# Performance work log

Hardware: AMD Instinct MI355X
Metric: run time of the kernel (lower is better)

Reference implementation:

```python
import jax, jax.numpy as jnp
import numpy as np

NUM_USERS = 100000
NUM_ITEMS = 50000
N_NODES = NUM_USERS + NUM_ITEMS
LATENT_DIM = 64
SBERT_DIM = 384
NUM_LAYERS = 3
N_EDGES = 2_000_000


def setup_inputs() -> dict:
    key = jax.random.key(0)
    k1, k2, k3, k4 = jax.random.split(key, 4)
    edge_index = jax.random.randint(k1, (2, N_EDGES), 0, N_NODES, dtype=jnp.int32)
    user_emb = jax.random.normal(k2, (NUM_USERS, LATENT_DIM), dtype=jnp.float32) * 0.1
    book_bert = jax.random.normal(k3, (NUM_ITEMS, SBERT_DIM), dtype=jnp.float32)
    # torch Linear weight layout: [out_features, in_features]
    w_proj = jax.random.normal(k4, (LATENT_DIM, SBERT_DIM), dtype=jnp.float32) * (1.0 / np.sqrt(SBERT_DIM))
    return {"edge_index": edge_index, "user_emb": user_emb, "book_bert": book_bert, "w_proj": w_proj}


def reference(edge_index, user_emb, book_bert, w_proj):
    src, dst = edge_index[0], edge_index[1]
    # initial embeddings: [users ; proj(book_bert)] -> [N, D]
    book_emb = book_bert @ w_proj.T
    emb0 = jnp.concatenate([user_emb, book_emb], axis=0)

    # symmetric gcn_norm without self-loops (PyG LGConv default)
    ones = jnp.ones((src.shape[0],), dtype=emb0.dtype)
    deg = jax.ops.segment_sum(ones, dst, num_segments=N_NODES)
    dis = jnp.where(deg > 0, jax.lax.rsqrt(jnp.maximum(deg, 1.0)), 0.0)
    norm = dis[src] * dis[dst]  # [E]

    x = emb0
    acc = emb0
    for _ in range(NUM_LAYERS):
        # out[dst] += norm * x[src]  (gather-scatter SpMM)
        msgs = norm[:, None] * x[src]  # [E, D]
        x = jax.ops.segment_sum(msgs, dst, num_segments=N_NODES)
        acc = acc + x
    out = acc / jnp.asarray(NUM_LAYERS + 1, dtype=emb0.dtype)
    return (emb0, out)
```

## Files before the change

kernel.cpp:

```cpp
#include <hip/hip_runtime.h>
#include <hip/hip_bf16.h>
#include <stdint.h>

#define NUM_USERS 100000
#define NUM_ITEMS 50000
#define N_NODES   150000
#define LATENT    64
#define SBERT     384
#define N_EDGES   2000000
#define OUT_OFF   (N_NODES * LATENT)
#define NBUCK     586
#define BCAP      4096
#define EPB       8192

typedef __hip_bfloat16 bf16;

__device__ __forceinline__ int ufl(int v) { return __builtin_amdgcn_readfirstlane(v); }

__global__ void k_zero_bcnt(int* __restrict__ bcnt) {
    int i = blockIdx.x * 256 + threadIdx.x;
    if (i < NBUCK) bcnt[i] = 0;
}

__global__ __launch_bounds__(256) void k_bin(const int* __restrict__ src,
                                             const int* __restrict__ dst,
                                             int* __restrict__ bcnt,
                                             unsigned* __restrict__ bin) {
    __shared__ int hist[NBUCK];
    __shared__ int base[NBUCK];
    const int tid = threadIdx.x;
    for (int i = tid; i < NBUCK; i += 256) hist[i] = 0;
    __syncthreads();
    const int e0 = blockIdx.x * EPB;
    const int e1 = min(e0 + EPB, N_EDGES);
    for (int e = e0 + tid; e < e1; e += 256)
        atomicAdd(&hist[dst[e] >> 8], 1);
    __syncthreads();
    for (int i = tid; i < NBUCK; i += 256) {
        int c = hist[i];
        base[i] = c ? atomicAdd(&bcnt[i], c) : 0;
        hist[i] = 0;
    }
    __syncthreads();
    for (int e = e0 + tid; e < e1; e += 256) {
        int d = dst[e];
        int b = d >> 8;
        int p = base[b] + atomicAdd(&hist[b], 1);
        bin[(size_t)b * BCAP + p] = (unsigned)src[e] | ((unsigned)(d & 255) << 18);
    }
}

__global__ __launch_bounds__(1024) void k_bscan(const int* __restrict__ bcnt,
                                                int* __restrict__ bbase) {
    __shared__ int sm[1024];
    int tid = threadIdx.x;
    int v = (tid < NBUCK) ? bcnt[tid] : 0;
    sm[tid] = v;
    __syncthreads();
    for (int off = 1; off < 1024; off <<= 1) {
        int t = (tid >= off) ? sm[tid - off] : 0;
        __syncthreads();
        sm[tid] += t;
        __syncthreads();
    }
    if (tid <= NBUCK) bbase[tid] = (tid == 0) ? 0 : sm[tid - 1];
}

__global__ __launch_bounds__(256) void k_build(const unsigned* __restrict__ bin,
                                               const int* __restrict__ bcnt,
                                               const int* __restrict__ bbase,
                                               int* __restrict__ rp,
                                               float* __restrict__ dis,
                                               int* __restrict__ cws) {
    __shared__ int h[256];
    __shared__ int lc[256];
    const int tid   = threadIdx.x;
    const int b     = blockIdx.x;
    const int nbase = b << 8;
    const unsigned* mybin = bin + (size_t)b * BCAP;
    h[tid] = 0;
    __syncthreads();
    const int cnt  = bcnt[b];
    const int base = bbase[b];
    for (int i = tid; i < cnt; i += 256)
        atomicAdd(&h[mybin[i] >> 18], 1);
    __syncthreads();
    int v = h[tid];
    __shared__ int sm[256];
    sm[tid] = v;
    __syncthreads();
    for (int off = 1; off < 256; off <<= 1) {
        int t = (tid >= off) ? sm[tid - off] : 0;
        __syncthreads();
        sm[tid] += t;
        __syncthreads();
    }
    int excl = sm[tid] - v;
    int n = nbase + tid;
    if (n < N_NODES) {
        rp[n]  = base + excl;
        dis[n] = (v > 0) ? rsqrtf((float)v) : 0.0f;
    }
    lc[tid] = base + excl;
    if (b == NBUCK - 1 && tid == 0) rp[N_NODES] = N_EDGES;
    __syncthreads();
    for (int i = tid; i < cnt; i += 256) {
        unsigned rec = mybin[i];
        int dl = rec >> 18;
        int pos = atomicAdd(&lc[dl], 1);
        cws[pos] = (int)(rec & 0x3FFFF);
    }
}

__global__ void k_copy_user(const float* __restrict__ u, const float* __restrict__ dis,
                            float* __restrict__ out, bf16* __restrict__ y) {
    int i = blockIdx.x * 256 + threadIdx.x;
    if (i < NUM_USERS * LATENT) {
        float v = u[i];
        out[i] = v;
        out[OUT_OFF + i] = v;
        float d = dis[i >> 6];
        y[i] = __float2bfloat16(d * v);
    }
}

__global__ __launch_bounds__(256) void k_proj(const float* __restrict__ bert,
                                              const float* __restrict__ w,
                                              const float* __restrict__ dis,
                                              float* __restrict__ out,
                                              bf16* __restrict__ y) {
    __shared__ float sB[128][33];
    __shared__ float sW[32][64];
    const int tid  = threadIdx.x;
    const int rb   = blockIdx.x * 128;
    const int col8 = (tid & 7) * 8;
    const int rowg = (tid >> 3) * 4;

    float acc[4][8];
#pragma unroll
    for (int i = 0; i < 4; ++i)
#pragma unroll
        for (int j = 0; j < 8; ++j) acc[i][j] = 0.0f;

    for (int kb = 0; kb < SBERT; kb += 32) {
        __syncthreads();
#pragma unroll
        for (int j = 0; j < 4; ++j) {
            int idx = tid + j * 256;
            int r  = idx >> 3;
            int k4 = (idx & 7) * 4;
            int rr = min(rb + r, NUM_ITEMS - 1);
            float4 v = *(const float4*)(bert + (size_t)rr * SBERT + kb + k4);
            sB[r][k4 + 0] = v.x; sB[r][k4 + 1] = v.y;
            sB[r][k4 + 2] = v.z; sB[r][k4 + 3] = v.w;
        }
#pragma unroll
        for (int j = 0; j < 2; ++j) {
            int idx = tid + j * 256;
            int c  = idx >> 3;
            int k4 = (idx & 7) * 4;
            float4 v = *(const float4*)(w + (size_t)c * SBERT + kb + k4);
            sW[k4 + 0][c] = v.x; sW[k4 + 1][c] = v.y;
            sW[k4 + 2][c] = v.z; sW[k4 + 3][c] = v.w;
        }
        __syncthreads();
#pragma unroll
        for (int kk = 0; kk < 32; ++kk) {
            float4 w0 = *(const float4*)&sW[kk][col8];
            float4 w1 = *(const float4*)&sW[kk][col8 + 4];
#pragma unroll
            for (int i = 0; i < 4; ++i) {
                float a = sB[rowg + i][kk];
                acc[i][0] = fmaf(a, w0.x, acc[i][0]);
                acc[i][1] = fmaf(a, w0.y, acc[i][1]);
                acc[i][2] = fmaf(a, w0.z, acc[i][2]);
                acc[i][3] = fmaf(a, w0.w, acc[i][3]);
                acc[i][4] = fmaf(a, w1.x, acc[i][4]);
                acc[i][5] = fmaf(a, w1.y, acc[i][5]);
                acc[i][6] = fmaf(a, w1.z, acc[i][6]);
                acc[i][7] = fmaf(a, w1.w, acc[i][7]);
            }
        }
    }
#pragma unroll
    for (int i = 0; i < 4; ++i) {
        int r = rb + rowg + i;
        if (r < NUM_ITEMS) {
            int n = NUM_USERS + r;
            size_t o = (size_t)n * LATENT + col8;
            float d = dis[n];
            float4 f0 = make_float4(acc[i][0], acc[i][1], acc[i][2], acc[i][3]);
            float4 f1 = make_float4(acc[i][4], acc[i][5], acc[i][6], acc[i][7]);
            *(float4*)(out + o)           = f0;
            *(float4*)(out + o + 4)       = f1;
            *(float4*)(out + OUT_OFF + o) = f0;
            *(float4*)(out + OUT_OFF + o + 4) = f1;
#pragma unroll
            for (int j = 0; j < 8; ++j) y[o + j] = __float2bfloat16(d * acc[i][j]);
        }
    }
}

template <bool FINAL>
__global__ __launch_bounds__(256) void k_spmm(const bf16* __restrict__ y,
                                              const int* __restrict__ rp,
                                              const int* __restrict__ cws,
                                              const float* __restrict__ dis,
                                              bf16* __restrict__ yn,
                                              float* __restrict__ acc) {
    int lane = threadIdx.x & 63;
    int node = ufl(blockIdx.x * 4 + (threadIdx.x >> 6));
    int beg = rp[node];
    int end = rp[node + 1];
    int last = end - 1;
    float a = 0.0f;
    for (int base = beg; base < end; base += 8) {
        int idx[8];
#pragma unroll
        for (int j = 0; j < 8; ++j)
            idx[j] = cws[min(base + j, last)];
        float v[8];
#pragma unroll
        for (int j = 0; j < 8; ++j)
            v[j] = __bfloat162float(y[(size_t)idx[j] * LATENT + lane]);
#pragma unroll
        for (int j = 0; j < 8; ++j)
            if (base + j <= last) a += v[j];
    }
    float d = dis[node];
    size_t o = (size_t)node * LATENT + lane;
    if (!FINAL) yn[o] = __float2bfloat16(d * d * a);
    float t = acc[o] + d * a;
    acc[o] = FINAL ? t * 0.25f : t;
}

extern "C" void kernel_launch(void* const* d_in, const int* in_sizes, int n_in,
                              void* d_out, int out_size, void* d_ws, size_t ws_size,
                              hipStream_t stream) {
    const int*   ei    = (const int*)d_in[0];
    const float* uemb  = (const float*)d_in[1];
    const float* bert  = (const float*)d_in[2];
    const float* wproj = (const float*)d_in[3];
    float* out = (float*)d_out;

    char* ws = (char*)d_ws;
    size_t off = 0;
    auto carve = [&](size_t bytes) -> void* {
        void* p = ws + off;
        off += (bytes + 255) & ~(size_t)255;
        return p;
    };
    float*    dis    = (float*)carve(sizeof(float) * N_NODES);
    int*      rp     = (int*)carve(sizeof(int) * (N_NODES + 1));
    int*      bcnt   = (int*)carve(sizeof(int) * NBUCK);
    int*      bbase  = (int*)carve(sizeof(int) * (NBUCK + 1));
    unsigned* bin    = (unsigned*)carve(sizeof(unsigned) * (size_t)NBUCK * BCAP);
    int*      cws    = (int*)carve(sizeof(int) * N_EDGES);
    bf16*     ye     = (bf16*)carve(sizeof(bf16) * (size_t)N_NODES * LATENT);
    bf16*     y0     = (bf16*)carve(sizeof(bf16) * (size_t)N_NODES * LATENT);
    bf16*     y1     = (bf16*)carve(sizeof(bf16) * (size_t)N_NODES * LATENT);

    const int* srcI = ei;
    const int* dstI = ei + N_EDGES;

    k_zero_bcnt<<<(NBUCK + 255) / 256, 256, 0, stream>>>(bcnt);
    k_bin<<<(N_EDGES + EPB - 1) / EPB, 256, 0, stream>>>(srcI, dstI, bcnt, bin);
    k_bscan<<<1, 1024, 0, stream>>>(bcnt, bbase);
    k_build<<<NBUCK, 256, 0, stream>>>(bin, bcnt, bbase, rp, dis, cws);
    k_copy_user<<<(NUM_USERS * LATENT + 255) / 256, 256, 0, stream>>>(uemb, dis, out, ye);
    k_proj<<<(NUM_ITEMS + 127) / 128, 256, 0, stream>>>(bert, wproj, dis, out, ye);

    float* accp = out + OUT_OFF;
    k_spmm<false><<<N_NODES / 4, 256, 0, stream>>>(ye, rp, cws, dis, y0, accp);
    k_spmm<false><<<N_NODES / 4, 256, 0, stream>>>(y0, rp, cws, dis, y1, accp);
    k_spmm<true ><<<N_NODES / 4, 256, 0, stream>>>(y1, rp, cws, dis, y0, accp);
}
```

Before: 463.6 us.

## Split bf16 embeddings into two feature halves and process each half per SpMM pass

The bf16 node features move from a [N,64] row layout into two [N,32] half-feature planes, and each SpMM layer now runs as two launches, one per half. Inside a launch the wave's two 32-lane halves each gather alternating edges and combine their sums with a cross-lane shuffle. The aim is to shrink the gathered working set per pass to 64-byte rows so it stays in cache better. In exchange the CSR index array is read twice as many times and the launch count doubles. The edge-binning block size also drops.

```diff
diff --git a/kernel.cpp b/kernel.cpp
--- a/kernel.cpp
+++ b/kernel.cpp
@@ -11,7 +11,8 @@
 #define OUT_OFF   (N_NODES * LATENT)
 #define NBUCK     586
 #define BCAP      4096
-#define EPB       8192
+#define EPB       2048
+#define YHALF     (N_NODES * 32)
 
 typedef __hip_bfloat16 bf16;
 
@@ -119,8 +120,10 @@
         float v = u[i];
         out[i] = v;
         out[OUT_OFF + i] = v;
-        float d = dis[i >> 6];
-        y[i] = __float2bfloat16(d * v);
+        int n = i >> 6;
+        int f = i & 63;
+        float d = dis[n];
+        y[(size_t)(f >> 5) * YHALF + (size_t)n * 32 + (f & 31)] = __float2bfloat16(d * v);
     }
 }
 
@@ -195,43 +198,51 @@
             *(float4*)(out + o + 4)       = f1;
             *(float4*)(out + OUT_OFF + o) = f0;
             *(float4*)(out + OUT_OFF + o + 4) = f1;
-#pragma unroll
-            for (int j = 0; j < 8; ++j) y[o + j] = __float2bfloat16(d * acc[i][j]);
+            size_t yo = (size_t)(col8 >> 5) * YHALF + (size_t)n * 32 + (col8 & 31);
+#pragma unroll
+            for (int j = 0; j < 8; ++j) y[yo + j] = __float2bfloat16(d * acc[i][j]);
         }
     }
 }
 
 template <bool FINAL>
-__global__ __launch_bounds__(256) void k_spmm(const bf16* __restrict__ y,
+__global__ __launch_bounds__(256) void k_spmm(const bf16* __restrict__ yh,
                                               const int* __restrict__ rp,
                                               const int* __restrict__ cws,
                                               const float* __restrict__ dis,
-                                              bf16* __restrict__ yn,
-                                              float* __restrict__ acc) {
+                                              bf16* __restrict__ ynh,
+                                              float* __restrict__ acch) {
     int lane = threadIdx.x & 63;
+    int par  = lane >> 5;
+    int feat = lane & 31;
     int node = ufl(blockIdx.x * 4 + (threadIdx.x >> 6));
     int beg = rp[node];
     int end = rp[node + 1];
     int last = end - 1;
+    float d = dis[node];
+    size_t o = (size_t)node * LATENT + feat;
+    float accv = acch[o];
     float a = 0.0f;
-    for (int base = beg; base < end; base += 8) {
+    for (int base = beg; base < end; base += 16) {
         int idx[8];
 #pragma unroll
         for (int j = 0; j < 8; ++j)
-            idx[j] = cws[min(base + j, last)];
+            idx[j] = cws[min(base + 2 * j + par, last)];
         float v[8];
 #pragma unroll
         for (int j = 0; j < 8; ++j)
-            v[j] = __bfloat162float(y[(size_t)idx[j] * LATENT + lane]);
+            v[j] = __bfloat162float(yh[(size_t)idx[j] * 32 + feat]);
 #pragma unroll
         for (int j = 0; j < 8; ++j)
-            if (base + j <= last) a += v[j];
-    }
-    float d = dis[node];
-    size_t o = (size_t)node * LATENT + lane;
-    if (!FINAL) yn[o] = __float2bfloat16(d * d * a);
-    float t = acc[o] + d * a;
-    acc[o] = FINAL ? t * 0.25f : t;
+            if (base + 2 * j + par <= last) a += v[j];
+    }
+    a += __shfl_xor(a, 32);
+    if (lane < 32) {
+        float t = accv + d * a;
+        acch[o] = FINAL ? t * 0.25f : t;
+    } else if (!FINAL) {
+        ynh[(size_t)node * 32 + feat] = __float2bfloat16(d * d * a);
+    }
 }
 
 extern "C" void kernel_launch(void* const* d_in, const int* in_sizes, int n_in,
@@ -271,7 +282,11 @@
     k_proj<<<(NUM_ITEMS + 127) / 128, 256, 0, stream>>>(bert, wproj, dis, out, ye);
 
     float* accp = out + OUT_OFF;
-    k_spmm<false><<<N_NODES / 4, 256, 0, stream>>>(ye, rp, cws, dis, y0, accp);
-    k_spmm<false><<<N_NODES / 4, 256, 0, stream>>>(y0, rp, cws, dis, y1, accp);
-    k_spmm<true ><<<N_NODES / 4, 256, 0, stream>>>(y1, rp, cws, dis, y0, accp);
-}
+    const int G = N_NODES / 4;
+    k_spmm<false><<<G, 256, 0, stream>>>(ye,         rp, cws, dis, y0,         accp);
+    k_spmm<false><<<G, 256, 0, stream>>>(ye + YHALF, rp, cws, dis, y0 + YHALF, accp + 32);
+    k_spmm<false><<<G, 256, 0, stream>>>(y0,         rp, cws, dis, y1,         accp);
+    k_spmm<false><<<G, 256, 0, stream>>>(y0 + YHALF, rp, cws, dis, y1 + YHALF, accp + 32);
+    k_spmm<true ><<<G, 256, 0, stream>>>(y1,         rp, cws, dis, y0,         accp);
+    k_spmm<true ><<<G, 256, 0, stream>>>(y1 + YHALF, rp, cws, dis, y0 + YHALF, accp + 32);
+}
```

Result: slower. 557.6 us (+20.3%).
